# Performance work log

Hardware: AMD Instinct MI355X
Metric: run time of the kernel (lower is better)

Reference implementation:

```python
import jax, jax.numpy as jnp
import numpy as np

EMBED_DIM = 4096
NUM_HEADS = 64
RANK = 1
B, T = 64, 64  # T must equal NUM_HEADS for the mask broadcast (faithful to source)


def setup_inputs() -> dict:
    key = jax.random.key(0)
    k1, k2, k3, k4, k5 = jax.random.split(key, 5)
    C = EMBED_DIM
    s = 0.02
    return {
        "x": jax.random.normal(k1, (B, T, C), dtype=jnp.float32),
        "W_atten": jax.random.normal(k2, (3 * C, C), dtype=jnp.float32) * s,
        "b_atten": jax.random.normal(k3, (3 * C,), dtype=jnp.float32) * s,
        "W_proj": jax.random.normal(k4, (C, C), dtype=jnp.float32) * s,
        "b_proj": jax.random.normal(k5, (C,), dtype=jnp.float32) * s,
    }


def reference(x, W_atten, b_atten, W_proj, b_proj):
    Bx, Tx, C = x.shape
    H = NUM_HEADS
    hd = C // H
    r = RANK
    qkv = jnp.einsum("btc,oc->bto", x, W_atten) + b_atten  # (B,T,3C)
    q, k, v = jnp.split(qkv, 3, axis=2)
    # view (B,T,rank,H,hd) then transpose(1,2) -> (B,rank,T,H,hd)
    def reshp(t):
        return t.reshape(Bx, Tx, r, H, hd).transpose(0, 2, 1, 3, 4)
    q, k, v = reshp(q), reshp(k), reshp(v)
    scale = (1.0 / np.sqrt(hd)) * (r ** 0.5)
    # attention across heads at each timestep: (B,rank,T,H,H)
    att = jnp.einsum("brtqd,brtkd->brtqk", q, k) * scale
    # tril[:T,:T] broadcasts onto trailing (H,H) dims (requires T == H)
    tril = jnp.tril(jnp.ones((Tx, Tx), dtype=jnp.float32))
    att = jnp.where(tril == 0, -jnp.inf, att)
    att = jax.nn.softmax(att, axis=-1)
    y = jnp.einsum("brtqk,brtkd->brtqd", att, v)  # (B,rank,T,H,hd)
    y = y.transpose(0, 2, 1, 3, 4).reshape(Bx, Tx, C)
    return jnp.einsum("btc,oc->bto", y, W_proj) + b_proj
```

## Files before the change

kernel.cpp:

```cpp
#include <hip/hip_runtime.h>
#include <stdint.h>

#define M_TOK   4096
#define C_DIM   4096
#define N_QKV   12288
#define KD      4096
#define NT2     32

typedef __bf16 bf16x8 __attribute__((ext_vector_type(8)));
typedef float  f32x4  __attribute__((ext_vector_type(4)));
typedef unsigned short ushort8 __attribute__((ext_vector_type(8)));

__device__ __forceinline__ unsigned short f2bf(float f) {
  unsigned int u = __builtin_bit_cast(unsigned int, f);
  u = (u + 0x7FFFu + ((u >> 16) & 1u)) >> 16;
  return (unsigned short)u;
}
__device__ __forceinline__ float bf2f(unsigned short h) {
  unsigned int u = ((unsigned int)h) << 16;
  return __builtin_bit_cast(float, u);
}

__global__ __launch_bounds__(256) void cvt_f32_bf16(const float* __restrict__ in,
                                                    unsigned short* __restrict__ out,
                                                    int n16) {
  int idx = blockIdx.x * 256 + threadIdx.x;
  if (idx >= n16) return;
  const float4* p = (const float4*)in;
  float4 a = p[idx * 2], b = p[idx * 2 + 1];
  uint4 r;
  r.x = (unsigned)f2bf(a.x) | ((unsigned)f2bf(a.y) << 16);
  r.y = (unsigned)f2bf(a.z) | ((unsigned)f2bf(a.w) << 16);
  r.z = (unsigned)f2bf(b.x) | ((unsigned)f2bf(b.y) << 16);
  r.w = (unsigned)f2bf(b.z) | ((unsigned)f2bf(b.w) << 16);
  ((uint4*)out)[idx] = r;
}

#define GLLDS(gp, lp) \
  __builtin_amdgcn_global_load_lds((const __attribute__((address_space(1))) unsigned int*)(gp), \
                                   (__attribute__((address_space(3))) unsigned int*)(lp), 16, 0, 0)


#define STAGE_A(buf, hf, tau) do {                                         \
    const unsigned short* g_ = Ag + (size_t)((hf) * 64) * KD + (tau) * 64; \
    unsigned short* d_ = As + (buf) * 16384 + (hf) * 8192 + t * 8;         \
    GLLDS(g_, d_);                                                         \
    GLLDS(g_ + (size_t)128 * KD, d_ + 4096);                               \
  } while (0)

#define STAGE_B(buf, nhf, tau) do {                                         \
    const unsigned short* g_ = Bg + (size_t)((nhf) * 32) * KD + (tau) * 64; \
    unsigned short* d_ = Bs + (buf) * 16384 + (nhf) * 8192 + t * 8;         \
    GLLDS(g_, d_);                                                          \
    GLLDS(g_ + (size_t)128 * KD, d_ + 4096);                                \
  } while (0)

#define LDA_(buf, mh) do {                                                        \
    const unsigned short* pa_ = As + (buf) * 16384 + (mh) * 8192 + wm * 4096 + lr * 64; \
    _Pragma("unroll") for (int mt_ = 0; mt_ < 4; ++mt_) {                         \
      afk[0][mt_] = *(const bf16x8*)(pa_ + mt_ * 1024 + ck0);                     \
      afk[1][mt_] = *(const bf16x8*)(pa_ + mt_ * 1024 + ck1);                     \
    }                                                                             \
  } while (0)

#define LDB_(buf, nhf, dst) do {                                                  \
    const unsigned short* pb_ = Bs + (buf) * 16384 + (nhf) * 8192 + wn * 2048 + lr * 64; \
    _Pragma("unroll") for (int nt_ = 0; nt_ < 2; ++nt_) {                         \
      dst[0][nt_] = *(const bf16x8*)(pb_ + nt_ * 1024 + ck0);                     \
      dst[1][nt_] = *(const bf16x8*)(pb_ + nt_ * 1024 + ck1);                     \
    }                                                                             \
  } while (0)

#define QUAD_(mh, nhf, bsrc) do {                                                 \
    _Pragma("unroll") for (int kk_ = 0; kk_ < 2; ++kk_)                           \
    _Pragma("unroll") for (int mt_ = 0; mt_ < 4; ++mt_)                           \
    _Pragma("unroll") for (int nt_ = 0; nt_ < 2; ++nt_)                           \
      acc[mh][nhf][mt_][nt_] = __builtin_amdgcn_mfma_f32_16x16x32_bf16(           \
          afk[kk_][mt_], bsrc[kk_][nt_], acc[mh][nhf][mt_][nt_], 0, 0, 0);        \
  } while (0)

#define PH_MID() do {                                      \
    asm volatile("" ::: "memory");                         \
    __builtin_amdgcn_s_barrier();                          \
    asm volatile("s_waitcnt lgkmcnt(0)" ::: "memory");     \
    __builtin_amdgcn_s_setprio(1);                         \
  } while (0)

#define PH_END() do {                                      \
    __builtin_amdgcn_s_setprio(0);                         \
    asm volatile("" ::: "memory");                         \
    __builtin_amdgcn_s_barrier();                          \
    asm volatile("" ::: "memory");                         \
  } while (0)

#define PH_END_VM() do {                                   \
    __builtin_amdgcn_s_setprio(0);                         \
    asm volatile("s_waitcnt vmcnt(6)" ::: "memory");       \
    __builtin_amdgcn_s_barrier();                          \
    asm volatile("" ::: "memory");                         \
  } while (0)

template <int OUT_BF16>
__global__ __launch_bounds__(512, 2) void gemm256(const unsigned short* __restrict__ A,
                                                  const unsigned short* __restrict__ B,
                                                  const float* __restrict__ bias,
                                                  void* __restrict__ Cptr,
                                                  int N) {
  __shared__ __align__(16) unsigned short As[32768];
  __shared__ __align__(16) unsigned short Bs[32768];

  const int t   = threadIdx.x;
  const int nwg = gridDim.x;
  const int bid = blockIdx.x;
  const int wg  = (bid & 7) * (nwg >> 3) + (bid >> 3);
  const int bm  = wg & 15;
  const int bn  = wg >> 4;

  const int w  = t >> 6, l = t & 63;
  const int wm = w >> 2, wn = w & 3;
  const int lr = l & 15, lq = l >> 4;
  const int ck0 = (lq ^ (lr & 7)) * 8;
  const int ck1 = ck0 ^ 32;

  const int r8  = t >> 3;
  const int kcs = ((t & 7) ^ (r8 & 7)) * 8;
  const unsigned short* Ag = A + (size_t)(bm * 256 + r8) * KD + kcs;
  const unsigned short* Bg = B + (size_t)(bn * 256 + ((t >> 8) << 6) + (r8 & 31)) * KD + kcs;

  f32x4 acc[2][2][4][2] = {};
  bf16x8 afk[2][4], bA[2][2], bB[2][2];

  STAGE_A(0, 0, 0); STAGE_B(0, 0, 0); STAGE_B(0, 1, 0); STAGE_A(0, 1, 0);
  STAGE_A(1, 0, 1); STAGE_B(1, 0, 1); STAGE_B(1, 1, 1);
  asm volatile("s_waitcnt vmcnt(6)" ::: "memory");
  __builtin_amdgcn_s_barrier();
  asm volatile("" ::: "memory");

#pragma unroll 1
  for (int i = 0; i < NT2; ++i) {
    const int t1 = 2 * i + 1;
    const int t2 = (2 * i + 2 < 64) ? 2 * i + 2 : 63;
    const int t3 = (2 * i + 3 < 64) ? 2 * i + 3 : 63;
    LDA_(0, 0); LDB_(0, 0, bA);
    STAGE_A(1, 1, t1);
    PH_MID(); QUAD_(0, 0, bA); PH_END();
    LDB_(0, 1, bB);
    STAGE_A(0, 0, t2);
    PH_MID(); QUAD_(0, 1, bB); PH_END();
    LDA_(0, 1);
    STAGE_B(0, 0, t2);
    PH_MID(); QUAD_(1, 0, bA); PH_END();
    STAGE_B(0, 1, t2);
    PH_MID(); QUAD_(1, 1, bB); PH_END_VM();
    LDA_(1, 0); LDB_(1, 0, bA);
    STAGE_A(0, 1, t2);
    PH_MID(); QUAD_(0, 0, bA); PH_END();
    LDB_(1, 1, bB);
    STAGE_A(1, 0, t3);
    PH_MID(); QUAD_(0, 1, bB); PH_END();
    LDA_(1, 1);
    STAGE_B(1, 0, t3);
    PH_MID(); QUAD_(1, 0, bA); PH_END();
    STAGE_B(1, 1, t3);
    PH_MID(); QUAD_(1, 1, bB); PH_END_VM();
  }

  asm volatile("s_waitcnt vmcnt(0)" ::: "memory");

  const int row0 = bm * 256 + wm * 128 + lq * 4;
  const int col0 = bn * 256 + wn * 64 + lr;
#pragma unroll
  for (int nhf = 0; nhf < 2; ++nhf)
#pragma unroll
    for (int nt = 0; nt < 2; ++nt) {
      const int col = col0 + nhf * 32 + nt * 16;
      const float bv = bias[col];
#pragma unroll
      for (int mh = 0; mh < 2; ++mh)
#pragma unroll
        for (int mt = 0; mt < 4; ++mt) {
          const int row = row0 + mh * 64 + mt * 16;
#pragma unroll
          for (int rg = 0; rg < 4; ++rg) {
            float v = acc[mh][nhf][mt][nt][rg] + bv;
            if (OUT_BF16)
              ((unsigned short*)Cptr)[(size_t)(row + rg) * N + col] = f2bf(v);
            else
              ((float*)Cptr)[(size_t)(row + rg) * N + col] = v;
          }
        }
    }
}

#define AST 72

__global__ __launch_bounds__(64) void attn_mfma(const unsigned short* __restrict__ qkv,
                                                unsigned short* __restrict__ y) {
  __shared__ __align__(16) unsigned short Ks[64 * AST];
  __shared__ __align__(16) unsigned short Vs[64 * AST];
  const int l  = threadIdx.x;
  const int lr = l & 15;
  const int lq = l >> 4;
  const size_t base = (size_t)blockIdx.x * 12288;

  {
    const int jr = l >> 3;
    const int cc = (l & 7) * 8;
#pragma unroll
    for (int c = 0; c < 8; ++c) {
      const int j = c * 8 + jr;
      *(uint4*)(Ks + j * AST + cc) = *(const uint4*)(qkv + base + 4096 + (size_t)j * 64 + cc);
      *(uint4*)(Vs + j * AST + cc) = *(const uint4*)(qkv + base + 8192 + (size_t)j * 64 + cc);
    }
  }

  bf16x8 aq[4][2];
#pragma unroll
  for (int it = 0; it < 4; ++it)
#pragma unroll
    for (int kk = 0; kk < 2; ++kk)
      aq[it][kk] = *(const bf16x8*)(qkv + base + (size_t)(it * 16 + lr) * 64 + kk * 32 + lq * 8);

  __syncthreads();

  f32x4 acc[4][4] = {};
#pragma unroll
  for (int kk = 0; kk < 2; ++kk) {
    bf16x8 bk[4];
#pragma unroll
    for (int jt = 0; jt < 4; ++jt)
      bk[jt] = *(const bf16x8*)(Ks + (jt * 16 + lr) * AST + kk * 32 + lq * 8);
#pragma unroll
    for (int it = 0; it < 4; ++it)
#pragma unroll
      for (int jt = 0; jt < 4; ++jt)
        acc[it][jt] = __builtin_amdgcn_mfma_f32_16x16x32_bf16(aq[it][kk], bk[jt], acc[it][jt], 0, 0, 0);
  }

#pragma unroll
  for (int it = 0; it < 4; ++it) {
#pragma unroll
    for (int rg = 0; rg < 4; ++rg) {
      const int row = it * 16 + lq * 4 + rg;
      float mx = -1e30f;
#pragma unroll
      for (int jt = 0; jt < 4; ++jt) {
        const int col = jt * 16 + lr;
        float s = acc[it][jt][rg] * 0.125f;
        s = (col <= row) ? s : -1e30f;
        acc[it][jt][rg] = s;
        mx = fmaxf(mx, s);
      }
#pragma unroll
      for (int d = 1; d < 16; d <<= 1)
        mx = fmaxf(mx, __shfl_xor(mx, d));
      float sum = 0.f;
#pragma unroll
      for (int jt = 0; jt < 4; ++jt) {
        float e = __expf(acc[it][jt][rg] - mx);
        acc[it][jt][rg] = e;
        sum += e;
      }
#pragma unroll
      for (int d = 1; d < 16; d <<= 1)
        sum += __shfl_xor(sum, d);
      const float inv = 1.f / sum;
#pragma unroll
      for (int jt = 0; jt < 4; ++jt)
        acc[it][jt][rg] *= inv;
    }
  }

#pragma unroll
  for (int it = 0; it < 4; ++it)
#pragma unroll
    for (int rg = 0; rg < 4; ++rg) {
      const int row = it * 16 + lq * 4 + rg;
#pragma unroll
      for (int jt = 0; jt < 4; ++jt)
        Ks[row * AST + jt * 16 + lr] = f2bf(acc[it][jt][rg]);
    }
  __syncthreads();

  f32x4 out[4][4] = {};
#pragma unroll
  for (int kk = 0; kk < 2; ++kk) {
    bf16x8 ap[4];
#pragma unroll
    for (int it = 0; it < 4; ++it)
      ap[it] = *(const bf16x8*)(Ks + (it * 16 + lr) * AST + kk * 32 + lq * 8);
#pragma unroll
    for (int dt = 0; dt < 4; ++dt) {
      ushort8 vt;
#pragma unroll
      for (int jj = 0; jj < 8; ++jj)
        vt[jj] = Vs[(kk * 32 + lq * 8 + jj) * AST + dt * 16 + lr];
      const bf16x8 bv = __builtin_bit_cast(bf16x8, vt);
#pragma unroll
      for (int it = 0; it < 4; ++it)
        out[it][dt] = __builtin_amdgcn_mfma_f32_16x16x32_bf16(ap[it], bv, out[it][dt], 0, 0, 0);
    }
  }

  unsigned short* yrow = y + (size_t)blockIdx.x * 4096;
#pragma unroll
  for (int it = 0; it < 4; ++it)
#pragma unroll
    for (int rg = 0; rg < 4; ++rg) {
      const int i = it * 16 + lq * 4 + rg;
#pragma unroll
      for (int dt = 0; dt < 4; ++dt)
        yrow[i * 64 + dt * 16 + lr] = f2bf(out[it][dt][rg]);
    }
}

extern "C" void kernel_launch(void* const* d_in, const int* in_sizes, int n_in,
                              void* d_out, int out_size, void* d_ws, size_t ws_size,
                              hipStream_t stream) {
  const float* x  = (const float*)d_in[0];
  const float* Wa = (const float*)d_in[1];
  const float* ba = (const float*)d_in[2];
  const float* Wp = (const float*)d_in[3];
  const float* bp = (const float*)d_in[4];
  float* out = (float*)d_out;

  unsigned short* regA = (unsigned short*)d_ws;
  unsigned short* regB = regA + (size_t)16777216;
  unsigned short* regC = regB + (size_t)50331648;
  unsigned short* xb   = regA;
  unsigned short* Wab  = regB;
  unsigned short* qkvb = regC;
  unsigned short* Wpb  = regA;
  unsigned short* yb   = regB;

  cvt_f32_bf16<<<(16777216 / 8) / 256, 256, 0, stream>>>(x, xb, 16777216 / 8);
  cvt_f32_bf16<<<(50331648 / 8) / 256, 256, 0, stream>>>(Wa, Wab, 50331648 / 8);

  gemm256<1><<<dim3((M_TOK / 256) * (N_QKV / 256)), dim3(512), 0, stream>>>(
      xb, Wab, ba, (void*)qkvb, N_QKV);

  cvt_f32_bf16<<<(16777216 / 8) / 256, 256, 0, stream>>>(Wp, Wpb, 16777216 / 8);

  attn_mfma<<<M_TOK, 64, 0, stream>>>(qkvb, yb);

  gemm256<0><<<dim3((M_TOK / 256) * (C_DIM / 256)), dim3(512), 0, stream>>>(
      yb, Wpb, bp, (void*)out, C_DIM);
}
```

Baseline: 961.2 us.

## Drop mid-phase barrier and lgkmcnt wait, interleave LDS reads with MFMAs

Restructures the GEMM main loop so each phase has a single barrier instead of two. The explicit lgkmcnt(0) wait before the MFMA block is gone, leaving the compiler free to interleave LDS fragment reads with MFMAs. Global-to-LDS staging is issued before the LDS reads, and A and B fragment loads are merged into one interleaved macro. This is meant to cut barrier stalls and hide LDS latency behind compute, but with fewer barriers there is a risk of LDS hazards between staging writes and other waves' reads.

```diff
diff --git a/kernel.cpp b/kernel.cpp
--- a/kernel.cpp
+++ b/kernel.cpp
@@ -15,10 +15,6 @@
   unsigned int u = __builtin_bit_cast(unsigned int, f);
   u = (u + 0x7FFFu + ((u >> 16) & 1u)) >> 16;
   return (unsigned short)u;
-}
-__device__ __forceinline__ float bf2f(unsigned short h) {
-  unsigned int u = ((unsigned int)h) << 16;
-  return __builtin_bit_cast(float, u);
 }
 
 __global__ __launch_bounds__(256) void cvt_f32_bf16(const float* __restrict__ in,
@@ -57,48 +53,58 @@
 
 #define LDA_(buf, mh) do {                                                        \
     const unsigned short* pa_ = As + (buf) * 16384 + (mh) * 8192 + wm * 4096 + lr * 64; \
-    _Pragma("unroll") for (int mt_ = 0; mt_ < 4; ++mt_) {                         \
-      afk[0][mt_] = *(const bf16x8*)(pa_ + mt_ * 1024 + ck0);                     \
-      afk[1][mt_] = *(const bf16x8*)(pa_ + mt_ * 1024 + ck1);                     \
-    }                                                                             \
+    afk[0][0] = *(const bf16x8*)(pa_ + 0 * 1024 + ck0);                           \
+    afk[0][1] = *(const bf16x8*)(pa_ + 1 * 1024 + ck0);                           \
+    afk[0][2] = *(const bf16x8*)(pa_ + 2 * 1024 + ck0);                           \
+    afk[0][3] = *(const bf16x8*)(pa_ + 3 * 1024 + ck0);                           \
+    afk[1][0] = *(const bf16x8*)(pa_ + 0 * 1024 + ck1);                           \
+    afk[1][1] = *(const bf16x8*)(pa_ + 1 * 1024 + ck1);                           \
+    afk[1][2] = *(const bf16x8*)(pa_ + 2 * 1024 + ck1);                           \
+    afk[1][3] = *(const bf16x8*)(pa_ + 3 * 1024 + ck1);                           \
   } while (0)
 
 #define LDB_(buf, nhf, dst) do {                                                  \
     const unsigned short* pb_ = Bs + (buf) * 16384 + (nhf) * 8192 + wn * 2048 + lr * 64; \
-    _Pragma("unroll") for (int nt_ = 0; nt_ < 2; ++nt_) {                         \
-      dst[0][nt_] = *(const bf16x8*)(pb_ + nt_ * 1024 + ck0);                     \
-      dst[1][nt_] = *(const bf16x8*)(pb_ + nt_ * 1024 + ck1);                     \
-    }                                                                             \
+    dst[0][0] = *(const bf16x8*)(pb_ + 0 * 1024 + ck0);                           \
+    dst[0][1] = *(const bf16x8*)(pb_ + 1 * 1024 + ck0);                           \
+    dst[1][0] = *(const bf16x8*)(pb_ + 0 * 1024 + ck1);                           \
+    dst[1][1] = *(const bf16x8*)(pb_ + 1 * 1024 + ck1);                           \
+  } while (0)
+
+#define LDAB_(buf, mh, nhf, dst) do {                                             \
+    const unsigned short* pa_ = As + (buf) * 16384 + (mh) * 8192 + wm * 4096 + lr * 64; \
+    const unsigned short* pb_ = Bs + (buf) * 16384 + (nhf) * 8192 + wn * 2048 + lr * 64; \
+    afk[0][0] = *(const bf16x8*)(pa_ + 0 * 1024 + ck0);                           \
+    afk[0][1] = *(const bf16x8*)(pa_ + 1 * 1024 + ck0);                           \
+    afk[0][2] = *(const bf16x8*)(pa_ + 2 * 1024 + ck0);                           \
+    afk[0][3] = *(const bf16x8*)(pa_ + 3 * 1024 + ck0);                           \
+    dst[0][0] = *(const bf16x8*)(pb_ + 0 * 1024 + ck0);                           \
+    dst[0][1] = *(const bf16x8*)(pb_ + 1 * 1024 + ck0);                           \
+    afk[1][0] = *(const bf16x8*)(pa_ + 0 * 1024 + ck1);                           \
+    afk[1][1] = *(const bf16x8*)(pa_ + 1 * 1024 + ck1);                           \
+    afk[1][2] = *(const bf16x8*)(pa_ + 2 * 1024 + ck1);                           \
+    afk[1][3] = *(const bf16x8*)(pa_ + 3 * 1024 + ck1);                           \
+    dst[1][0] = *(const bf16x8*)(pb_ + 0 * 1024 + ck1);                           \
+    dst[1][1] = *(const bf16x8*)(pb_ + 1 * 1024 + ck1);                           \
   } while (0)
 
 #define QUAD_(mh, nhf, bsrc) do {                                                 \
+    __builtin_amdgcn_s_setprio(1);                                                \
     _Pragma("unroll") for (int kk_ = 0; kk_ < 2; ++kk_)                           \
     _Pragma("unroll") for (int mt_ = 0; mt_ < 4; ++mt_)                           \
     _Pragma("unroll") for (int nt_ = 0; nt_ < 2; ++nt_)                           \
       acc[mh][nhf][mt_][nt_] = __builtin_amdgcn_mfma_f32_16x16x32_bf16(           \
           afk[kk_][mt_], bsrc[kk_][nt_], acc[mh][nhf][mt_][nt_], 0, 0, 0);        \
-  } while (0)
-
-#define PH_MID() do {                                      \
-    asm volatile("" ::: "memory");                         \
-    __builtin_amdgcn_s_barrier();                          \
-    asm volatile("s_waitcnt lgkmcnt(0)" ::: "memory");     \
-    __builtin_amdgcn_s_setprio(1);                         \
-  } while (0)
-
-#define PH_END() do {                                      \
-    __builtin_amdgcn_s_setprio(0);                         \
+    __builtin_amdgcn_s_setprio(0);                                                \
+  } while (0)
+
+#define BAR_() do {                                        \
     asm volatile("" ::: "memory");                         \
     __builtin_amdgcn_s_barrier();                          \
     asm volatile("" ::: "memory");                         \
   } while (0)
 
-#define PH_END_VM() do {                                   \
-    __builtin_amdgcn_s_setprio(0);                         \
-    asm volatile("s_waitcnt vmcnt(6)" ::: "memory");       \
-    __builtin_amdgcn_s_barrier();                          \
-    asm volatile("" ::: "memory");                         \
-  } while (0)
+#define VM6_() asm volatile("s_waitcnt vmcnt(6)" ::: "memory")
 
 template <int OUT_BF16>
 __global__ __launch_bounds__(512, 2) void gemm256(const unsigned short* __restrict__ A,
@@ -132,37 +138,46 @@
 
   STAGE_A(0, 0, 0); STAGE_B(0, 0, 0); STAGE_B(0, 1, 0); STAGE_A(0, 1, 0);
   STAGE_A(1, 0, 1); STAGE_B(1, 0, 1); STAGE_B(1, 1, 1);
-  asm volatile("s_waitcnt vmcnt(6)" ::: "memory");
-  __builtin_amdgcn_s_barrier();
-  asm volatile("" ::: "memory");
+  VM6_();
+  BAR_();
 
 #pragma unroll 1
   for (int i = 0; i < NT2; ++i) {
     const int t1 = 2 * i + 1;
     const int t2 = (2 * i + 2 < 64) ? 2 * i + 2 : 63;
     const int t3 = (2 * i + 3 < 64) ? 2 * i + 3 : 63;
-    LDA_(0, 0); LDB_(0, 0, bA);
     STAGE_A(1, 1, t1);
-    PH_MID(); QUAD_(0, 0, bA); PH_END();
+    LDAB_(0, 0, 0, bA);
+    QUAD_(0, 0, bA);
+    BAR_();
+    STAGE_A(0, 0, t2);
     LDB_(0, 1, bB);
-    STAGE_A(0, 0, t2);
-    PH_MID(); QUAD_(0, 1, bB); PH_END();
+    QUAD_(0, 1, bB);
+    BAR_();
+    STAGE_B(0, 0, t2);
     LDA_(0, 1);
-    STAGE_B(0, 0, t2);
-    PH_MID(); QUAD_(1, 0, bA); PH_END();
+    QUAD_(1, 0, bA);
+    BAR_();
     STAGE_B(0, 1, t2);
-    PH_MID(); QUAD_(1, 1, bB); PH_END_VM();
-    LDA_(1, 0); LDB_(1, 0, bA);
+    QUAD_(1, 1, bB);
+    VM6_();
+    BAR_();
     STAGE_A(0, 1, t2);
-    PH_MID(); QUAD_(0, 0, bA); PH_END();
+    LDAB_(1, 0, 0, bA);
+    QUAD_(0, 0, bA);
+    BAR_();
+    STAGE_A(1, 0, t3);
     LDB_(1, 1, bB);
-    STAGE_A(1, 0, t3);
-    PH_MID(); QUAD_(0, 1, bB); PH_END();
+    QUAD_(0, 1, bB);
+    BAR_();
+    STAGE_B(1, 0, t3);
     LDA_(1, 1);
-    STAGE_B(1, 0, t3);
-    PH_MID(); QUAD_(1, 0, bA); PH_END();
+    QUAD_(1, 0, bA);
+    BAR_();
     STAGE_B(1, 1, t3);
-    PH_MID(); QUAD_(1, 1, bB); PH_END_VM();
+    QUAD_(1, 1, bB);
+    VM6_();
+    BAR_();
   }
 
   asm volatile("s_waitcnt vmcnt(0)" ::: "memory");
```

After: 950.9 us. About the same (-1.1%).
